# Optimization experiments

Hardware: AMD Instinct MI355X
Metric: run time of the kernel (lower is better)

## Reference

```python
import jax, jax.numpy as jnp
import numpy as np

NUM_BUCKETS = 32
MAX_DISTANCE = 128
NUM_HEADS = 16
D_KV = 64


def _relative_position_bucket(relative_position):
    # bidirectional buckets, faithful to T5Attention._relative_position_bucket
    num_buckets = NUM_BUCKETS // 2
    relative_buckets = (relative_position > 0).astype(jnp.int32) * num_buckets
    relative_position = jnp.abs(relative_position)
    max_exact = num_buckets // 2
    is_small = relative_position < max_exact
    rp_f = relative_position.astype(jnp.float32)
    rel_if_large = max_exact + (
        jnp.log(rp_f / max_exact) / np.log(MAX_DISTANCE / max_exact) * (num_buckets - max_exact)
    )
    rel_if_large = jnp.minimum(rel_if_large, num_buckets - 1)
    relative_buckets = relative_buckets + jnp.where(is_small, rp_f, rel_if_large).astype(jnp.int32)
    return relative_buckets


def setup_inputs() -> dict:
    key = jax.random.key(0)
    ks = jax.random.split(key, 6)
    B, S, D = 2, 2048, 1024
    inner = NUM_HEADS * D_KV  # 1024
    q_std = (inner * D_KV) ** (-0.5)
    kv_std = inner ** (-0.5)
    return {
        "hidden_states": jax.random.normal(ks[0], (B, S, D), jnp.float32),
        "attention_mask": jnp.ones((B, S), jnp.int32),
        "Wq": jax.random.normal(ks[1], (D, inner), jnp.float32) * q_std,
        "Wk": jax.random.normal(ks[2], (D, inner), jnp.float32) * kv_std,
        "Wv": jax.random.normal(ks[3], (D, inner), jnp.float32) * kv_std,
        "Wo": jax.random.normal(ks[4], (inner, D), jnp.float32) * kv_std,
        "rel_bias": jax.random.normal(ks[5], (NUM_BUCKETS, NUM_HEADS), jnp.float32),
    }


def reference(hidden_states, attention_mask, Wq, Wk, Wv, Wo, rel_bias):
    B, S, D = hidden_states.shape
    H, Dk = NUM_HEADS, D_KV

    q = (hidden_states @ Wq).reshape(B, S, H, Dk)
    k = (hidden_states @ Wk).reshape(B, S, H, Dk)
    v = (hidden_states @ Wv).reshape(B, S, H, Dk)
    q = q / jnp.sqrt(jnp.asarray(Dk, q.dtype))

    scores = jnp.einsum('bthd,bshd->bhts', q, k)  # [B,H,S,S]

    # relative position bias
    pos = jnp.arange(S, dtype=jnp.int32)
    rel_pos = pos[None, :] - pos[:, None]          # memory - context, [S,S]
    buckets = _relative_position_bucket(rel_pos)   # [S,S]
    bias = rel_bias[buckets]                       # [S,S,H]
    scores = scores + bias.transpose(2, 0, 1)[None].astype(scores.dtype)

    mask = attention_mask[:, None, None, :].astype(scores.dtype)
    scores = scores + (1.0 - mask) * jnp.finfo(scores.dtype).min

    attn = jax.nn.softmax(scores, axis=-1)
    out = jnp.einsum('bhts,bshd->bthd', attn, v).reshape(B, S, H * Dk)
    return out @ Wo
```

## Files before the change

### kernel.cpp

```cpp
#include <hip/hip_runtime.h>
#include <hip/hip_bf16.h>
#include <math.h>

typedef __attribute__((ext_vector_type(8))) short bf16x8;
typedef __attribute__((ext_vector_type(4))) short s16x4;
typedef __attribute__((ext_vector_type(4))) float f32x4;

constexpr int cB = 2, cS = 2048, cH = 16, cD = 64, cIn = 1024, cM = 1024;
constexpr float cLog2e = 1.4426950408889634f;

union BfPack { bf16x8 v; short s[8]; };
union BfPack4 { s16x4 v; short s[4]; };

__device__ __forceinline__ short f2bf(float f) {
    union { float f; unsigned u; } v; v.f = f;
    unsigned r = v.u + 0x7fffu + ((v.u >> 16) & 1u);
    return (short)(r >> 16);
}

__device__ __forceinline__ f32x4 mfma16(bf16x8 a, bf16x8 b, f32x4 c) {
    return __builtin_amdgcn_mfma_f32_16x16x32_bf16(a, b, c, 0, 0, 0);
}

__device__ __forceinline__ void async16(const short* g, short* l) {
    __builtin_amdgcn_global_load_lds(
        (const __attribute__((address_space(1))) unsigned*)(uintptr_t)g,
        (__attribute__((address_space(3))) unsigned*)(uintptr_t)l, 16, 0, 0);
}

__global__ void bias_table_kernel(const float* __restrict__ rel_bias,
                                  const int* __restrict__ mask,
                                  float* __restrict__ bt,
                                  float* __restrict__ maskadd) {
    int idx = blockIdx.x * blockDim.x + threadIdx.x;
    if (idx < 4096) maskadd[idx] = (1.0f - (float)mask[idx]) * -3.0e38f;
    if (idx >= 4095) return;
    int delta = idx - 2047;
    int rb = (delta > 0) ? 16 : 0;
    int ar = delta < 0 ? -delta : delta;
    int bucket;
    if (ar < 8) {
        bucket = rb + ar;
    } else {
        float rl = 8.0f + logf((float)ar * 0.125f) * 2.8853900817779268f;
        rl = fminf(rl, 15.0f);
        bucket = rb + (int)rl;
    }
    #pragma unroll
    for (int h = 0; h < cH; h++)
        bt[h * 4096 + 2048 + delta] = rel_bias[bucket * cH + h] * cLog2e;
}

__global__ __launch_bounds__(256) void conv_hidden_kernel(
    const float* __restrict__ h, short* __restrict__ hbf) {
    int t = blockIdx.x * 256 + threadIdx.x;
    const float4* src = (const float4*)h;
    float4 a = src[2 * t], b = src[2 * t + 1];
    BfPack p;
    p.s[0] = f2bf(a.x); p.s[1] = f2bf(a.y); p.s[2] = f2bf(a.z); p.s[3] = f2bf(a.w);
    p.s[4] = f2bf(b.x); p.s[5] = f2bf(b.y); p.s[6] = f2bf(b.z); p.s[7] = f2bf(b.w);
    ((bf16x8*)hbf)[t] = p.v;
}

__global__ __launch_bounds__(256) void conv_wt_kernel(
    const float* __restrict__ Wq, const float* __restrict__ Wk,
    const float* __restrict__ Wv, const float* __restrict__ Wo,
    short* __restrict__ Wt) {
    const int z = blockIdx.z;
    const float* W = (z == 0) ? Wq : (z == 1) ? Wk : (z == 2) ? Wv : Wo;
    const float scale = (z == 0) ? 0.125f * cLog2e : 1.0f;
    const int n0 = blockIdx.x * 64, k0 = blockIdx.y * 64;
    __shared__ short sW[64][72];
    const int t = threadIdx.x;
    const int r = t >> 2, c4 = (t & 3) * 16;
    {
        const float* src = W + (size_t)(k0 + r) * cM + n0 + c4;
        BfPack p[2];
        #pragma unroll
        for (int q = 0; q < 2; q++) {
            float4 x = ((const float4*)src)[2 * q];
            float4 y = ((const float4*)src)[2 * q + 1];
            p[q].s[0] = f2bf(x.x * scale); p[q].s[1] = f2bf(x.y * scale);
            p[q].s[2] = f2bf(x.z * scale); p[q].s[3] = f2bf(x.w * scale);
            p[q].s[4] = f2bf(y.x * scale); p[q].s[5] = f2bf(y.y * scale);
            p[q].s[6] = f2bf(y.z * scale); p[q].s[7] = f2bf(y.w * scale);
        }
        *(bf16x8*)&sW[r][c4] = p[0].v;
        *(bf16x8*)&sW[r][c4 + 8] = p[1].v;
    }
    __syncthreads();
    const int n = t >> 2, kc = (t & 3) * 16;
    BfPack o0, o1;
    #pragma unroll
    for (int j = 0; j < 8; j++) o0.s[j] = sW[kc + j][n];
    #pragma unroll
    for (int j = 0; j < 8; j++) o1.s[j] = sW[kc + 8 + j][n];
    short* dst = Wt + (size_t)z * cM * cIn + (size_t)(n0 + n) * cIn + k0 + kc;
    *(bf16x8*)dst = o0.v;
    *(bf16x8*)(dst + 8) = o1.v;
}

template <bool SWAP>
__device__ __forceinline__ void gemm_core(
    const short* __restrict__ A, const short* __restrict__ Bt,
    short* smem, int m0, int c0, int tid, f32x4 (&acc)[4][4]) {
    short* sA = smem;
    short* sB = smem + 4096;
    const int w = tid >> 6, l = tid & 63;
    const int m16 = l & 15, g = l >> 4;
    const int srow = l >> 2, scol = (l & 3) * 8;
    const int mq = (w & 1) * 64, nq = (w >> 1) * 64;

    for (int k0 = 0; k0 < cIn; k0 += 32) {
        __syncthreads();
        async16(A + (size_t)(m0 + w * 16 + srow) * cIn + k0 + scol,
                sA + w * 512 + l * 8);
        async16(A + (size_t)(m0 + 64 + w * 16 + srow) * cIn + k0 + scol,
                sA + 2048 + w * 512 + l * 8);
        async16(Bt + (size_t)(c0 + w * 16 + srow) * cIn + k0 + scol,
                sB + w * 512 + l * 8);
        async16(Bt + (size_t)(c0 + 64 + w * 16 + srow) * cIn + k0 + scol,
                sB + 2048 + w * 512 + l * 8);
        __syncthreads();
        bf16x8 af[4], bf[4];
        #pragma unroll
        for (int i = 0; i < 4; i++)
            af[i] = *(const bf16x8*)(sA + (mq + i * 16 + m16) * 32 + g * 8);
        #pragma unroll
        for (int j = 0; j < 4; j++)
            bf[j] = *(const bf16x8*)(sB + (nq + j * 16 + m16) * 32 + g * 8);
        #pragma unroll
        for (int i = 0; i < 4; i++)
            #pragma unroll
            for (int j = 0; j < 4; j++)
                acc[i][j] = SWAP ? mfma16(bf[j], af[i], acc[i][j])
                                 : mfma16(af[i], bf[j], acc[i][j]);
    }
}

__global__ __launch_bounds__(256) void gemm_qkv_kernel(
    const short* __restrict__ hbf, const short* __restrict__ Wt,
    short* __restrict__ Qrm, short* __restrict__ Krm, short* __restrict__ VT) {
    const int z = blockIdx.z;
    const short* Bt = Wt + (size_t)z * cM * cIn;
    const int m0 = blockIdx.y * 128, c0 = blockIdx.x * 128;
    __shared__ short smem[8192];
    const int tid = threadIdx.x, w = tid >> 6, l = tid & 63;
    const int m16 = l & 15, g = l >> 4;
    const int mq = (w & 1) * 64, nq = (w >> 1) * 64;
    f32x4 acc[4][4] = {};

    if (z <= 1) {
        gemm_core<false>(hbf, Bt, smem, m0, c0, tid, acc);
        short* dst = (z == 0) ? Qrm : Krm;
        #pragma unroll
        for (int i = 0; i < 4; i++)
            #pragma unroll
            for (int j = 0; j < 4; j++)
                #pragma unroll
                for (int r = 0; r < 4; r++)
                    dst[(size_t)(m0 + mq + i * 16 + g * 4 + r) * cM +
                        c0 + nq + j * 16 + m16] = f2bf(acc[i][j][r]);
    } else {
        gemm_core<true>(hbf, Bt, smem, m0, c0, tid, acc);
        #pragma unroll
        for (int i = 0; i < 4; i++) {
            const int srow_g = m0 + mq + i * 16 + m16;
            const int bb = srow_g >> 11, ss = srow_g & 2047;
            #pragma unroll
            for (int j = 0; j < 4; j++)
                #pragma unroll
                for (int r = 0; r < 4; r++) {
                    const int wcol = c0 + nq + j * 16 + g * 4 + r;
                    VT[(((size_t)bb * cH + (wcol >> 6)) * cD + (wcol & 63)) * cS
                       + ss] = f2bf(acc[i][j][r]);
                }
        }
    }
}

__global__ __launch_bounds__(256) void attn_kernel(
    const short* __restrict__ Qrm, const short* __restrict__ Krm,
    const short* __restrict__ VT, const float* __restrict__ maskadd,
    const float* __restrict__ bias_t, short* __restrict__ ctx) {
    const int b = blockIdx.z, h = blockIdx.y;
    const int q0 = blockIdx.x * 64;
    const short* VTp = VT + ((size_t)b * cH + h) * cS * cD;
    const float* bh = bias_t + h * 4096 + 2048;
    const float* mp = maskadd + b * cS;

    const int tid = threadIdx.x;
    const int wave = tid >> 6, lane = tid & 63;
    const int m16 = lane & 15, g = lane >> 4;

    __shared__ short Kt[64][72];
    __shared__ short Vt[64][72];

    const int q = q0 + wave * 16 + m16;
    const short* qb = Qrm + (size_t)(b * cS + q) * cM + h * cD;
    bf16x8 qf0 = *(const bf16x8*)(qb + g * 8);
    bf16x8 qf1 = *(const bf16x8*)(qb + 32 + g * 8);

    f32x4 o[4] = {};
    f32x4 lacc = {};
    BfPack ones;
    #pragma unroll
    for (int i = 0; i < 8; i++) ones.s[i] = (short)0x3F80;

    const int srow = tid >> 3;
    const int scol = (tid & 7) << 3;
    const int kb = ((scol >> 4) & 1) * 32 + ((scol >> 3) & 1) * 16 +
                   ((scol >> 5) & 1) * 4;
    const short* kbase = Krm + (size_t)b * cS * cM + h * cD;

    bf16x8 kr0 = *(const bf16x8*)(kbase + (size_t)srow * cM + scol);
    bf16x8 kr1 = *(const bf16x8*)(kbase + (size_t)(srow + 32) * cM + scol);
    bf16x8 vr0 = *(const bf16x8*)(VTp + (size_t)srow * cS + scol);
    bf16x8 vr1 = *(const bf16x8*)(VTp + (size_t)(srow + 32) * cS + scol);

    for (int kt = 0; kt < cS; kt += 64) {
        __syncthreads();
        *(bf16x8*)&Kt[srow][scol] = kr0;
        *(bf16x8*)&Kt[srow + 32][scol] = kr1;
        {
            BfPack v0, v1; v0.v = vr0; v1.v = vr1;
            BfPack4 a, b2, c, d;
            #pragma unroll
            for (int i = 0; i < 4; i++) { a.s[i] = v0.s[i]; b2.s[i] = v0.s[4 + i]; }
            #pragma unroll
            for (int i = 0; i < 4; i++) { c.s[i] = v1.s[i]; d.s[i] = v1.s[4 + i]; }
            *(s16x4*)&Vt[srow][kb]          = a.v;
            *(s16x4*)&Vt[srow][kb + 8]      = b2.v;
            *(s16x4*)&Vt[srow + 32][kb]     = c.v;
            *(s16x4*)&Vt[srow + 32][kb + 8] = d.v;
        }
        __syncthreads();

        const int ktn = (kt + 64 < cS) ? kt + 64 : 0;
        kr0 = *(const bf16x8*)(kbase + (size_t)(ktn + srow) * cM + scol);
        kr1 = *(const bf16x8*)(kbase + (size_t)(ktn + srow + 32) * cM + scol);
        vr0 = *(const bf16x8*)(VTp + (size_t)srow * cS + ktn + scol);
        vr1 = *(const bf16x8*)(VTp + (size_t)(srow + 32) * cS + ktn + scol);

        f32x4 s[4];
        #pragma unroll
        for (int st = 0; st < 4; st++) {
            const int keyb = kt + st * 16 + g * 4;
            f32x4 init;
            #pragma unroll
            for (int c = 0; c < 4; c++)
                init[c] = bh[keyb + c - q] + mp[keyb + c];
            bf16x8 klo = *(const bf16x8*)&Kt[st * 16 + m16][g * 8];
            bf16x8 khi = *(const bf16x8*)&Kt[st * 16 + m16][32 + g * 8];
            s[st] = mfma16(khi, qf1, mfma16(klo, qf0, init));
        }

        BfPack pp[2];
        #pragma unroll
        for (int st = 0; st < 4; st++) {
            #pragma unroll
            for (int r = 0; r < 2; r++) {
                float p0 = __builtin_amdgcn_exp2f(s[st][2 * r]);
                float p1 = __builtin_amdgcn_exp2f(s[st][2 * r + 1]);
                __hip_bfloat162 h2 = __float22bfloat162_rn(float2{p0, p1});
                short2 sp = *(short2*)&h2;
                pp[st & 1].s[(st >> 1) * 4 + 2 * r]     = sp.x;
                pp[st & 1].s[(st >> 1) * 4 + 2 * r + 1] = sp.y;
            }
        }

        lacc = mfma16(ones.v, pp[0].v, lacc);
        lacc = mfma16(ones.v, pp[1].v, lacc);

        #pragma unroll
        for (int nt = 0; nt < 4; nt++) {
            bf16x8 vlo = *(const bf16x8*)&Vt[nt * 16 + m16][g * 8];
            bf16x8 vhi = *(const bf16x8*)&Vt[nt * 16 + m16][32 + g * 8];
            o[nt] = mfma16(vlo, pp[0].v, o[nt]);
            o[nt] = mfma16(vhi, pp[1].v, o[nt]);
        }
    }

    const float inv = 1.0f / lacc[0];
    short* cb = ctx + ((size_t)b * cS + q) * cM + h * cD;
    #pragma unroll
    for (int nt = 0; nt < 4; nt++) {
        BfPack4 pk;
        #pragma unroll
        for (int r = 0; r < 4; r++) pk.s[r] = f2bf(o[nt][r] * inv);
        *(s16x4*)(cb + nt * 16 + g * 4) = pk.v;
    }
}

__global__ __launch_bounds__(256) void gemm_o_kernel(
    const short* __restrict__ ctx, const short* __restrict__ WoT,
    float* __restrict__ out) {
    const int m0 = blockIdx.y * 128, c0 = blockIdx.x * 128;
    __shared__ short smem[8192];
    const int tid = threadIdx.x, w = tid >> 6, l = tid & 63;
    const int m16 = l & 15, g = l >> 4;
    const int mq = (w & 1) * 64, nq = (w >> 1) * 64;
    f32x4 acc[4][4] = {};
    gemm_core<false>(ctx, WoT, smem, m0, c0, tid, acc);
    #pragma unroll
    for (int i = 0; i < 4; i++)
        #pragma unroll
        for (int j = 0; j < 4; j++)
            #pragma unroll
            for (int r = 0; r < 4; r++)
                out[(size_t)(m0 + mq + i * 16 + g * 4 + r) * cM +
                    c0 + nq + j * 16 + m16] = acc[i][j][r];
}

extern "C" void kernel_launch(void* const* d_in, const int* in_sizes, int n_in,
                              void* d_out, int out_size, void* d_ws, size_t ws_size,
                              hipStream_t stream) {
    const float* hidden   = (const float*)d_in[0];
    const int*   mask     = (const int*)d_in[1];
    const float* Wq       = (const float*)d_in[2];
    const float* Wk       = (const float*)d_in[3];
    const float* Wv       = (const float*)d_in[4];
    const float* Wo       = (const float*)d_in[5];
    const float* rel_bias = (const float*)d_in[6];
    float* out = (float*)d_out;

    short* hbf_ctx = (short*)d_ws;
    short* Wt  = hbf_ctx + (size_t)4 * 1024 * 1024;
    short* Qrm = Wt  + (size_t)4 * 1024 * 1024;
    short* Krm = Qrm + (size_t)4 * 1024 * 1024;
    short* VT  = Krm + (size_t)4 * 1024 * 1024;
    float* bias_t  = (float*)(VT + (size_t)4 * 1024 * 1024);
    float* maskf   = bias_t + 16 * 4096;

    bias_table_kernel<<<16, 256, 0, stream>>>(rel_bias, mask, bias_t, maskf);
    conv_hidden_kernel<<<2048, 256, 0, stream>>>(hidden, hbf_ctx);
    conv_wt_kernel<<<dim3(16, 16, 4), 256, 0, stream>>>(Wq, Wk, Wv, Wo, Wt);
    gemm_qkv_kernel<<<dim3(8, 32, 3), 256, 0, stream>>>(hbf_ctx, Wt, Qrm, Krm, VT);
    attn_kernel<<<dim3(32, cH, cB), 256, 0, stream>>>(Qrm, Krm, VT, maskf, bias_t,
                                                      hbf_ctx);
    gemm_o_kernel<<<dim3(8, 32), 256, 0, stream>>>(hbf_ctx, Wt + (size_t)3 * 1024 * 1024,
                                                   out);
}
```

Baseline: 213.2 us.

## Double-buffer K/V tiles with async global-to-LDS loads and XOR swizzle

The attention kernel now stages K and V tiles into a double-buffered LDS region using async global-to-LDS copies. Each next tile is issued before the current one is computed, which removes the register staging and one of the two barriers per iteration. V is stored pre-permuted in the projection kernel so no in-kernel shuffle is needed. An XOR swizzle replaces the padded layout to avoid bank conflicts. The cost is twice the LDS, and correctness depends on async16 completing before the single barrier at the end of each iteration.

New measurement: 234.5 us. 10.0% more time.

```diff
diff --git a/kernel.cpp b/kernel.cpp
--- a/kernel.cpp
+++ b/kernel.cpp
@@ -167,13 +167,16 @@
         for (int i = 0; i < 4; i++) {
             const int srow_g = m0 + mq + i * 16 + m16;
             const int bb = srow_g >> 11, ss = srow_g & 2047;
+            const int s6 = ss & 63;
+            const int kap = (s6 & 3) | ((s6 & 28) << 1) | ((s6 >> 3) & 4);
+            const int col = (ss & ~63) + kap;
             #pragma unroll
             for (int j = 0; j < 4; j++)
                 #pragma unroll
                 for (int r = 0; r < 4; r++) {
                     const int wcol = c0 + nq + j * 16 + g * 4 + r;
                     VT[(((size_t)bb * cH + (wcol >> 6)) * cD + (wcol & 63)) * cS
-                       + ss] = f2bf(acc[i][j][r]);
+                       + col] = f2bf(acc[i][j][r]);
                 }
         }
     }
@@ -181,11 +184,11 @@
 
 __global__ __launch_bounds__(256) void attn_kernel(
     const short* __restrict__ Qrm, const short* __restrict__ Krm,
-    const short* __restrict__ VT, const float* __restrict__ maskadd,
+    const short* __restrict__ VTK, const float* __restrict__ maskadd,
     const float* __restrict__ bias_t, short* __restrict__ ctx) {
     const int b = blockIdx.z, h = blockIdx.y;
     const int q0 = blockIdx.x * 64;
-    const short* VTp = VT + ((size_t)b * cH + h) * cS * cD;
+    const short* VTp = VTK + ((size_t)b * cH + h) * cS * cD;
     const float* bh = bias_t + h * 4096 + 2048;
     const float* mp = maskadd + b * cS;
 
@@ -193,8 +196,8 @@
     const int wave = tid >> 6, lane = tid & 63;
     const int m16 = lane & 15, g = lane >> 4;
 
-    __shared__ short Kt[64][72];
-    __shared__ short Vt[64][72];
+    __shared__ short Kt[2][64][64];
+    __shared__ short Vt[2][64][64];
 
     const int q = q0 + wave * 16 + m16;
     const short* qb = Qrm + (size_t)(b * cS + q) * cM + h * cD;
@@ -207,40 +210,35 @@
     #pragma unroll
     for (int i = 0; i < 8; i++) ones.s[i] = (short)0x3F80;
 
-    const int srow = tid >> 3;
-    const int scol = (tid & 7) << 3;
-    const int kb = ((scol >> 4) & 1) * 32 + ((scol >> 3) & 1) * 16 +
-                   ((scol >> 5) & 1) * 4;
+    const int row0 = wave * 8 + (lane >> 3);
+    const int row1 = row0 + 32;
+    const int u = lane & 7;
     const short* kbase = Krm + (size_t)b * cS * cM + h * cD;
-
-    bf16x8 kr0 = *(const bf16x8*)(kbase + (size_t)srow * cM + scol);
-    bf16x8 kr1 = *(const bf16x8*)(kbase + (size_t)(srow + 32) * cM + scol);
-    bf16x8 vr0 = *(const bf16x8*)(VTp + (size_t)srow * cS + scol);
-    bf16x8 vr1 = *(const bf16x8*)(VTp + (size_t)(srow + 32) * cS + scol);
+    const short* srcK0 = kbase + (size_t)row0 * cM + ((u ^ (row0 & 7)) << 3);
+    const short* srcK1 = kbase + (size_t)row1 * cM + ((u ^ (row1 & 7)) << 3);
+    const short* srcV0 = VTp + (size_t)row0 * cS + ((u ^ (row0 & 7)) << 3);
+    const short* srcV1 = VTp + (size_t)row1 * cS + ((u ^ (row1 & 7)) << 3);
+    short* dK0 = (short*)Kt + wave * 512 + lane * 8;
+    short* dV0 = (short*)Vt + wave * 512 + lane * 8;
+
+    const int koff = m16 * 64 + ((g ^ (m16 & 7)) << 3);
+
+    async16(srcK0, dK0);
+    async16(srcK1, dK0 + 2048);
+    async16(srcV0, dV0);
+    async16(srcV1, dV0 + 2048);
+    __syncthreads();
 
     for (int kt = 0; kt < cS; kt += 64) {
-        __syncthreads();
-        *(bf16x8*)&Kt[srow][scol] = kr0;
-        *(bf16x8*)&Kt[srow + 32][scol] = kr1;
-        {
-            BfPack v0, v1; v0.v = vr0; v1.v = vr1;
-            BfPack4 a, b2, c, d;
-            #pragma unroll
-            for (int i = 0; i < 4; i++) { a.s[i] = v0.s[i]; b2.s[i] = v0.s[4 + i]; }
-            #pragma unroll
-            for (int i = 0; i < 4; i++) { c.s[i] = v1.s[i]; d.s[i] = v1.s[4 + i]; }
-            *(s16x4*)&Vt[srow][kb]          = a.v;
-            *(s16x4*)&Vt[srow][kb + 8]      = b2.v;
-            *(s16x4*)&Vt[srow + 32][kb]     = c.v;
-            *(s16x4*)&Vt[srow + 32][kb + 8] = d.v;
-        }
-        __syncthreads();
-
-        const int ktn = (kt + 64 < cS) ? kt + 64 : 0;
-        kr0 = *(const bf16x8*)(kbase + (size_t)(ktn + srow) * cM + scol);
-        kr1 = *(const bf16x8*)(kbase + (size_t)(ktn + srow + 32) * cM + scol);
-        vr0 = *(const bf16x8*)(VTp + (size_t)srow * cS + ktn + scol);
-        vr1 = *(const bf16x8*)(VTp + (size_t)(srow + 32) * cS + ktn + scol);
+        const int cur = (kt >> 6) & 1, nxt = cur ^ 1;
+        if (kt + 64 < cS) {
+            async16(srcK0 + (size_t)(kt + 64) * cM, dK0 + nxt * 4096);
+            async16(srcK1 + (size_t)(kt + 64) * cM, dK0 + nxt * 4096 + 2048);
+            async16(srcV0 + kt + 64, dV0 + nxt * 4096);
+            async16(srcV1 + kt + 64, dV0 + nxt * 4096 + 2048);
+        }
+        const short* KtC = (const short*)Kt + cur * 4096;
+        const short* VtC = (const short*)Vt + cur * 4096;
 
         f32x4 s[4];
         #pragma unroll
@@ -250,8 +248,8 @@
             #pragma unroll
             for (int c = 0; c < 4; c++)
                 init[c] = bh[keyb + c - q] + mp[keyb + c];
-            bf16x8 klo = *(const bf16x8*)&Kt[st * 16 + m16][g * 8];
-            bf16x8 khi = *(const bf16x8*)&Kt[st * 16 + m16][32 + g * 8];
+            bf16x8 klo = *(const bf16x8*)(KtC + st * 1024 + koff);
+            bf16x8 khi = *(const bf16x8*)(KtC + st * 1024 + (koff ^ 32));
             s[st] = mfma16(khi, qf1, mfma16(klo, qf0, init));
         }
 
@@ -274,11 +272,13 @@
 
         #pragma unroll
         for (int nt = 0; nt < 4; nt++) {
-            bf16x8 vlo = *(const bf16x8*)&Vt[nt * 16 + m16][g * 8];
-            bf16x8 vhi = *(const bf16x8*)&Vt[nt * 16 + m16][32 + g * 8];
+            bf16x8 vlo = *(const bf16x8*)(VtC + nt * 1024 + koff);
+            bf16x8 vhi = *(const bf16x8*)(VtC + nt * 1024 + (koff ^ 32));
             o[nt] = mfma16(vlo, pp[0].v, o[nt]);
             o[nt] = mfma16(vhi, pp[1].v, o[nt]);
         }
+
+        __syncthreads();
     }
 
     const float inv = 1.0f / lacc[0];
```
